# Kernel optimization log

Measured on AMD Instinct MI355X. Metric: run time of the kernel, lower is better.

Reference implementation:

```python
import jax, jax.numpy as jnp
import numpy as np

B, P, C = 64, 196, 768   # batch, num_patches, hidden_size
HS = 384                 # hidden_s (token-mixing hidden dim)
NG = 8                   # num_grids
GMIN, GMAX = -1.0, 1.0


def _rbf(x):
    # fast-KAN radial basis: exp(-((x - grid_i)/denom)^2), grid over [GMIN, GMAX]
    grid = jnp.linspace(GMIN, GMAX, NG).astype(x.dtype)
    denom = (GMAX - GMIN) / (NG - 1)
    return jnp.exp(-jnp.square((x[..., None] - grid) / denom))  # [..., din, NG]


def _kan_linear(x, spline_w, base_w, base_b):
    # x: [..., din]; spline_w: [dout, din*NG]; base_w: [dout, din]; base_b: [dout]
    basis = _rbf(x).reshape(*x.shape[:-1], -1)          # [..., din*NG]
    out = basis @ spline_w.T                            # spline term (no bias)
    out = out + jax.nn.silu(x) @ base_w.T + base_b      # base update term
    return out


def setup_inputs() -> dict:
    key = jax.random.key(0)
    ks = jax.random.split(key, 5)
    s = 0.1  # spline_weight_init_scale
    return {
        "x": jax.random.normal(ks[0], (B, P, C), jnp.float32),
        "fc1_spline_w": jax.random.normal(ks[1], (HS, P * NG), jnp.float32) * (s / np.sqrt(P * NG)),
        "fc1_base_w": jax.random.normal(ks[2], (HS, P), jnp.float32) / np.sqrt(P),
        "fc1_base_b": jnp.zeros((HS,), jnp.float32),
        "fc2_spline_w": jax.random.normal(ks[3], (P, HS * NG), jnp.float32) * (s / np.sqrt(HS * NG)),
        "fc2_base_w": jax.random.normal(ks[4], (P, HS), jnp.float32) / np.sqrt(HS),
        "fc2_base_b": jnp.zeros((P,), jnp.float32),
    }


def reference(x, fc1_spline_w, fc1_base_w, fc1_base_b,
              fc2_spline_w, fc2_base_w, fc2_base_b):
    skip_param = 1.0
    # token mixing: permute so KANLinear acts over the patch axis
    h = jnp.swapaxes(x, 1, 2)                                   # [B, C, P]
    h = _kan_linear(h, fc1_spline_w, fc1_base_w, fc1_base_b)    # [B, C, HS]
    # dropout p=0 -> identity; the two intermediate permutes cancel
    h = _kan_linear(h, fc2_spline_w, fc2_base_w, fc2_base_b)    # [B, C, P]
    out = jnp.swapaxes(h, 1, 2)                                 # [B, P, C]
    return out + skip_param * x
```

## Files before the change

### kernel.cpp

```cpp
#include <hip/hip_runtime.h>
#include <cstdint>

#define B_  64
#define P_  196
#define C_  768
#define HS_ 384
#define M_  49152
#define RT_ 96
#define NB_ (M_ / RT_)

#define NC1 13
#define KT1 111
#define NT1 12
#define NC2 24
#define KT2 216
#define NT2 7

#define H1_ELEMS  ((size_t)M_ * HS_)
#define W1P_ELEMS ((size_t)KT1 * NT1 * 512)
#define W2P_ELEMS ((size_t)KT2 * NT2 * 512)
#define PACK_G1   (W1P_ELEMS / 8)
#define PACK_G    ((W1P_ELEMS + W2P_ELEMS) / 8)

typedef __attribute__((ext_vector_type(8)))  short short8;
typedef __attribute__((ext_vector_type(16))) float f32x16;
typedef __attribute__((ext_vector_type(2)))  float float2v;

#define MFMA(w, a, c) __builtin_amdgcn_mfma_f32_32x32x16_bf16((w), (a), (c), 0, 0, 0)

static __device__ __forceinline__ float bf2f(unsigned short u) {
    union { unsigned int i; float f; } v; v.i = ((unsigned int)u) << 16; return v.f;
}
static __device__ __forceinline__ unsigned short f2bf_rne(float f) {
    union { float f; unsigned int i; } v; v.f = f;
    unsigned int r = v.i + 0x7FFFu + ((v.i >> 16) & 1u);
    return (unsigned short)(r >> 16);
}
static __device__ __forceinline__ unsigned int pack2(float a, float b) {
    unsigned int ua = __float_as_uint(a) + 0x8000u;
    unsigned int ub = __float_as_uint(b) + 0x8000u;
    return __builtin_amdgcn_perm(ub, ua, 0x07060302u);
}
static __device__ __forceinline__ short8 rbf8(float s) {
    const float Rr = 1.2011224087864498f;
    const float Aa = 4.2039284307525743f;
    float t1 = __builtin_fmaf(Aa, s, Aa);
    float2v t2 = {t1, t1};
    union { short8 s8; unsigned int u[4]; } r;
#pragma unroll
    for (int q = 0; q < 4; q++) {
        float2v c = {(float)(2 * q) * Rr, (float)(2 * q + 1) * Rr};
        float2v u = t2 - c;
        float2v m = -(u * u);
        r.u[q] = pack2(__builtin_amdgcn_exp2f(m[0]),
                       __builtin_amdgcn_exp2f(m[1]));
    }
    return r.s8;
}
static __device__ __forceinline__ unsigned int silu2(float a, float b) {
    const float L2E = 1.4426950408889634f;
    float2v v = {a, b};
    float2v t = v * (-L2E);
    float2v e = {__builtin_amdgcn_exp2f(t[0]), __builtin_amdgcn_exp2f(t[1])};
    float2v den = e + (float2v){1.f, 1.f};
    float2v rc = {__builtin_amdgcn_rcpf(den[0]), __builtin_amdgcn_rcpf(den[1])};
    float2v f = v * rc;
    return pack2(f[0], f[1]);
}

static __device__ __forceinline__ void block_sync_lds() {
    __builtin_amdgcn_sched_barrier(0);
    asm volatile("s_waitcnt lgkmcnt(0)" ::: "memory");
    __builtin_amdgcn_s_barrier();
    __builtin_amdgcn_sched_barrier(0);
}

static __device__ __forceinline__ void cvt8(const float4 a, const float4 b,
                                            unsigned short* o) {
    o[0] = f2bf_rne(a.x); o[1] = f2bf_rne(a.y); o[2] = f2bf_rne(a.z); o[3] = f2bf_rne(a.w);
    o[4] = f2bf_rne(b.x); o[5] = f2bf_rne(b.y); o[6] = f2bf_rne(b.z); o[7] = f2bf_rne(b.w);
}

__global__ void pack_w_kernel(const float* __restrict__ w1s,
                              const float* __restrict__ w1b,
                              const float* __restrict__ w2s,
                              const float* __restrict__ w2b,
                              unsigned short* __restrict__ w1p,
                              unsigned short* __restrict__ w2p) {
    int g = blockIdx.x * 256 + threadIdx.x;
    if (g >= PACK_G) return;
    union { short8 s8; unsigned short u[8]; } ov;
    if (g < PACK_G1) {
        int lane = g & 63;
        int lin  = g >> 6;
        int nt   = lin % NT1;
        int tt   = lin / NT1;
        int cc   = (tt < 108) ? tt / 9 : 12;
        int kk   = (tt < 108) ? tt % 9 : (tt - 108);
        int ktl  = (cc < 12) ? kk : ((kk < 2) ? kk : 8);
        int n = nt * 32 + (lane & 31);
        int khalf = lane >> 5;
        if (ktl < 8) {
            int p = cc * 16 + ktl * 2 + khalf;
            const float4* src = (const float4*)(w1s + (size_t)n * 1568 + (size_t)p * 8);
            cvt8(src[0], src[1], ov.u);
        } else {
            int p0 = cc * 16 + khalf * 8;
            if (p0 + 7 < P_) {
                const float4* src = (const float4*)(w1b + (size_t)n * 196 + p0);
                cvt8(src[0], src[1], ov.u);
            } else {
#pragma unroll
                for (int j = 0; j < 8; j++) {
                    int p = p0 + j;
                    float v = (p < P_) ? w1b[(size_t)n * 196 + p] : 0.f;
                    ov.u[j] = f2bf_rne(v);
                }
            }
        }
        *(short8*)&w1p[(size_t)g * 8] = ov.s8;
    } else {
        int g2 = g - PACK_G1;
        int lane = g2 & 63;
        int lin  = g2 >> 6;
        int nt   = lin % NT2;
        int tt   = lin / NT2;
        int cc   = tt / 9;
        int ktl  = tt % 9;
        int n = nt * 32 + (lane & 31);
        int khalf = lane >> 5;
        if (n < P_) {
            if (ktl < 8) {
                int s = cc * 16 + ktl * 2 + khalf;
                const float4* src = (const float4*)(w2s + (size_t)n * 3072 + (size_t)s * 8);
                cvt8(src[0], src[1], ov.u);
            } else {
                int s0 = cc * 16 + khalf * 8;
                const float4* src = (const float4*)(w2b + (size_t)n * 384 + s0);
                cvt8(src[0], src[1], ov.u);
            }
        } else {
#pragma unroll
            for (int j = 0; j < 8; j++) ov.u[j] = f2bf_rne(0.f);
        }
        *(short8*)&w2p[(size_t)g2 * 8] = ov.s8;
    }
}

#define TS_  1536
#define FB_  (9 * TS_)

__global__ __launch_bounds__(256, 2)
void fc1_kernel(const float* __restrict__ x,
                const unsigned short* __restrict__ w1p,
                const float* __restrict__ b1,
                unsigned short* __restrict__ h1t) {
    __shared__ __align__(16) unsigned short frag[2 * FB_];
    int blk = blockIdx.x;
    int tid = threadIdx.x;
    int b   = blk >> 3;
    int c0  = (blk & 7) * RT_;
    const float* xb = x + (size_t)b * (P_ * C_);

    int colA = tid & 63, scA = tid >> 6;
    int colB = 64 + (tid & 31), scB = tid >> 5;
    int pbase_rbfA  = ((colA >> 5) << 9) + (colA & 31) * 8;
    int pbase_rbfB  = 1024 + (colB & 31) * 8;
    int pbase_siluA = 8 * TS_ + ((colA >> 5) << 9) + ((scA >> 1) << 8) + (colA & 31) * 8 + (scA & 1) * 4;
    int pbase_siluB = 8 * TS_ + 1024 + ((scB >> 2) << 8) + (colB & 31) * 8 + (scB & 3) * 2;

    int wave = tid >> 6, lane = tid & 63;
    int l31 = lane & 31, half = lane >> 5;
    int nt0 = wave * 3;

    f32x16 acc[3][3];
#pragma unroll
    for (int rt = 0; rt < 3; rt++)
#pragma unroll
        for (int nt = 0; nt < 3; nt++)
#pragma unroll
            for (int i = 0; i < 16; i++) acc[rt][nt][i] = 0.f;

    const short8* wp = (const short8*)w1p;
    short8 wbuf[2][3];

    auto wload = [&](int d, const short8* wt0, int kk) {
        const short8* wt = wt0 + (size_t)kk * (NT1 * 64);
        wbuf[d][0] = wt[0]; wbuf[d][1] = wt[64]; wbuf[d][2] = wt[128];
    };
    auto do_mfma = [&](short8 w0, short8 w1, short8 w2,
                       short8 a0, short8 a1, short8 a2) {
        acc[0][0] = MFMA(w0, a0, acc[0][0]); acc[1][0] = MFMA(w0, a1, acc[1][0]); acc[2][0] = MFMA(w0, a2, acc[2][0]);
        acc[0][1] = MFMA(w1, a0, acc[0][1]); acc[1][1] = MFMA(w1, a1, acc[1][1]); acc[2][1] = MFMA(w1, a2, acc[2][1]);
        acc[0][2] = MFMA(w2, a0, acc[0][2]); acc[1][2] = MFMA(w2, a1, acc[1][2]); acc[2][2] = MFMA(w2, a2, acc[2][2]);
    };
    auto produce = [&](int fb, const float (&ra)[4], const float (&rb2)[2]) {
#pragma unroll
        for (int i = 0; i < 4; i++) {
            int sl = scA * 4 + i;
            *(short8*)&frag[fb + (sl >> 1) * TS_ + ((sl & 1) << 8) + pbase_rbfA] = rbf8(ra[i]);
        }
#pragma unroll
        for (int i = 0; i < 2; i++) {
            int sl = scB * 2 + i;
            *(short8*)&frag[fb + (sl >> 1) * TS_ + ((sl & 1) << 8) + pbase_rbfB] = rbf8(rb2[i]);
        }
        uint2 sv;
        sv.x = silu2(ra[0], ra[1]);
        sv.y = silu2(ra[2], ra[3]);
        *(uint2*)&frag[fb + pbase_siluA] = sv;
        *(unsigned int*)&frag[fb + pbase_siluB] = silu2(rb2[0], rb2[1]);
    };
    auto body = [&](int cc, const float (&rbPA)[4], const float (&rbPB)[2],
                    float (&rbLA)[4], float (&rbLB)[2]) {
        const short8* wt0 = wp + ((size_t)(cc * 9) * NT1 + nt0) * 64 + lane;
        wload(0, wt0, 0); wload(1, wt0, 1);
        int fbP = ((cc + 1) & 1) * FB_;
        const unsigned short* fg = &frag[(cc & 1) * FB_];
        short8 a0 = *(const short8*)&fg[lane * 8];
        short8 a1 = *(const short8*)&fg[512 + lane * 8];
        short8 a2 = *(const short8*)&fg[1024 + lane * 8];
#pragma unroll
        for (int kk = 0; kk < 9; kk++) {
            short8 na0, na1, na2;
            if (kk < 8) {
                na0 = *(const short8*)&fg[(kk + 1) * TS_ + lane * 8];
                na1 = *(const short8*)&fg[(kk + 1) * TS_ + 512 + lane * 8];
                na2 = *(const short8*)&fg[(kk + 1) * TS_ + 1024 + lane * 8];
            }
            short8 w0 = wbuf[kk & 1][0], w1 = wbuf[kk & 1][1], w2 = wbuf[kk & 1][2];
            if (kk < 7) wload(kk & 1, wt0, kk + 2);
            if (kk < 4) {
                int sl = scA * 4 + kk;
                *(short8*)&frag[fbP + (sl >> 1) * TS_ + ((sl & 1) << 8) + pbase_rbfA] = rbf8(rbPA[kk]);
            } else if (kk == 4) {
#pragma unroll
                for (int i = 0; i < 2; i++) {
                    int sl = scB * 2 + i;
                    *(short8*)&frag[fbP + (sl >> 1) * TS_ + ((sl & 1) << 8) + pbase_rbfB] = rbf8(rbPB[i]);
                }
            } else if (kk == 5) {
                uint2 sv;
                sv.x = silu2(rbPA[0], rbPA[1]);
                sv.y = silu2(rbPA[2], rbPA[3]);
                *(uint2*)&frag[fbP + pbase_siluA] = sv;
                *(unsigned int*)&frag[fbP + pbase_siluB] = silu2(rbPB[0], rbPB[1]);
            } else if (kk == 6) {
#pragma unroll
                for (int i = 0; i < 2; i++) {
                    int p = (cc + 2) * 16 + scA * 4 + i;
                    p = (p < P_) ? p : (P_ - 1);
                    rbLA[i] = xb[(size_t)p * C_ + c0 + colA];
                }
            } else if (kk == 7) {
#pragma unroll
                for (int i = 2; i < 4; i++) {
                    int p = (cc + 2) * 16 + scA * 4 + i;
                    p = (p < P_) ? p : (P_ - 1);
                    rbLA[i] = xb[(size_t)p * C_ + c0 + colA];
                }
            } else {
#pragma unroll
                for (int i = 0; i < 2; i++) {
                    int p = (cc + 2) * 16 + scB * 2 + i;
                    p = (p < P_) ? p : (P_ - 1);
                    rbLB[i] = xb[(size_t)p * C_ + c0 + colB];
                }
            }
            do_mfma(w0, w1, w2, a0, a1, a2);
            if (kk < 8) { a0 = na0; a1 = na1; a2 = na2; }
        }
        block_sync_lds();
    };

    float rbA_A[4], rbB_A[4], rbA_B[2], rbB_B[2];
#pragma unroll
    for (int i = 0; i < 4; i++) {
        rbA_A[i] = xb[(size_t)(scA * 4 + i) * C_ + c0 + colA];
        rbB_A[i] = xb[(size_t)(16 + scA * 4 + i) * C_ + c0 + colA];
    }
#pragma unroll
    for (int i = 0; i < 2; i++) {
        rbA_B[i] = xb[(size_t)(scB * 2 + i) * C_ + c0 + colB];
        rbB_B[i] = xb[(size_t)(16 + scB * 2 + i) * C_ + c0 + colB];
    }
    produce(0, rbA_A, rbA_B);
    block_sync_lds();

    for (int c2 = 0; c2 < 6; c2++) {
        body(2 * c2,     rbB_A, rbB_B, rbA_A, rbA_B);
        body(2 * c2 + 1, rbA_A, rbA_B, rbB_A, rbB_B);
    }
    {
        const short8* wt0 = wp + ((size_t)108 * NT1 + nt0) * 64 + lane;
        wload(0, wt0, 0); wload(1, wt0, 1);
        const unsigned short* fg = &frag[0];
#pragma unroll
        for (int kk = 0; kk < 3; kk++) {
            short8 w0 = wbuf[kk & 1][0], w1 = wbuf[kk & 1][1], w2 = wbuf[kk & 1][2];
            if (kk == 0) wload(0, wt0, 2);
            int ktl = (kk < 2) ? kk : 8;
            short8 a0 = *(const short8*)&fg[ktl * TS_ + lane * 8];
            short8 a1 = *(const short8*)&fg[ktl * TS_ + 512 + lane * 8];
            short8 a2 = *(const short8*)&fg[ktl * TS_ + 1024 + lane * 8];
            do_mfma(w0, w1, w2, a0, a1, a2);
        }
    }

#pragma unroll
    for (int nt = 0; nt < 3; nt++) {
        int n0 = (nt0 + nt) * 32 + 4 * half;
#pragma unroll
        for (int reg = 0; reg < 16; reg++) {
            int n = n0 + (reg & 3) + 8 * (reg >> 2);
            float bv = b1[n];
#pragma unroll
            for (int rt = 0; rt < 3; rt++) {
                h1t[(size_t)n * M_ + blk * RT_ + rt * 32 + l31] = f2bf_rne(acc[rt][nt][reg] + bv);
            }
        }
    }
}

__global__ __launch_bounds__(256, 2)
void fc2_kernel(const unsigned short* __restrict__ h1t,
                const unsigned short* __restrict__ w2p,
                const float* __restrict__ b2,
                const float* __restrict__ x,
                float* __restrict__ out) {
    __shared__ __align__(16) unsigned short frag[2 * FB_];
    int blk = blockIdx.x;
    int tid = threadIdx.x;
    int rbase = blk * RT_;

    int colA = tid & 63, scA = tid >> 6;
    int colB = 64 + (tid & 31), scB = tid >> 5;
    int pbase_rbfA  = ((colA >> 5) << 9) + (colA & 31) * 8;
    int pbase_rbfB  = 1024 + (colB & 31) * 8;
    int pbase_siluA = 8 * TS_ + ((colA >> 5) << 9) + ((scA >> 1) << 8) + (colA & 31) * 8 + (scA & 1) * 4;
    int pbase_siluB = 8 * TS_ + 1024 + ((scB >> 2) << 8) + (colB & 31) * 8 + (scB & 3) * 2;

    int wave = tid >> 6, lane = tid & 63;
    int l31 = lane & 31, half = lane >> 5;
    int nt0 = wave * 2;
    int ntn = (wave < 3) ? 2 : 1;
    int off1 = (ntn > 1) ? 64 : 0;

    f32x16 acc[3][2];
#pragma unroll
    for (int rt = 0; rt < 3; rt++)
#pragma unroll
        for (int nt = 0; nt < 2; nt++)
#pragma unroll
            for (int i = 0; i < 16; i++) acc[rt][nt][i] = 0.f;

    const short8* wp = (const short8*)w2p;
    short8 wbuf[2][2];

    auto wload = [&](int d, const short8* wt0, int kk) {
        const short8* wt = wt0 + (size_t)kk * (NT2 * 64);
        wbuf[d][0] = wt[0]; wbuf[d][1] = wt[off1];
    };
    auto do_mfma = [&](short8 w0, short8 w1, short8 a0, short8 a1, short8 a2) {
        acc[0][0] = MFMA(w0, a0, acc[0][0]); acc[1][0] = MFMA(w0, a1, acc[1][0]); acc[2][0] = MFMA(w0, a2, acc[2][0]);
        if (ntn == 2) {
            acc[0][1] = MFMA(w1, a0, acc[0][1]); acc[1][1] = MFMA(w1, a1, acc[1][1]); acc[2][1] = MFMA(w1, a2, acc[2][1]);
        }
    };
    auto produce = [&](int fb, const unsigned short (&ra)[4], const unsigned short (&rb2)[2]) {
        float v0 = bf2f(ra[0]), v1 = bf2f(ra[1]), v2 = bf2f(ra[2]), v3 = bf2f(ra[3]);
        float u0 = bf2f(rb2[0]), u1 = bf2f(rb2[1]);
        float vv[4] = {v0, v1, v2, v3};
#pragma unroll
        for (int i = 0; i < 4; i++) {
            int sl = scA * 4 + i;
            *(short8*)&frag[fb + (sl >> 1) * TS_ + ((sl & 1) << 8) + pbase_rbfA] = rbf8(vv[i]);
        }
        float uu[2] = {u0, u1};
#pragma unroll
        for (int i = 0; i < 2; i++) {
            int sl = scB * 2 + i;
            *(short8*)&frag[fb + (sl >> 1) * TS_ + ((sl & 1) << 8) + pbase_rbfB] = rbf8(uu[i]);
        }
        uint2 sv;
        sv.x = silu2(v0, v1);
        sv.y = silu2(v2, v3);
        *(uint2*)&frag[fb + pbase_siluA] = sv;
        *(unsigned int*)&frag[fb + pbase_siluB] = silu2(u0, u1);
    };
    auto body = [&](int cc, const unsigned short (&rbPA)[4], const unsigned short (&rbPB)[2],
                    unsigned short (&rbLA)[4], unsigned short (&rbLB)[2]) {
        bool doProd = (cc + 1 < NC2);
        const short8* wt0 = wp + ((size_t)(cc * 9) * NT2 + nt0) * 64 + lane;
        wload(0, wt0, 0); wload(1, wt0, 1);
        int fbP = ((cc + 1) & 1) * FB_;
        const unsigned short* fg = &frag[(cc & 1) * FB_];
        short8 a0 = *(const short8*)&fg[lane * 8];
        short8 a1 = *(const short8*)&fg[512 + lane * 8];
        short8 a2 = *(const short8*)&fg[1024 + lane * 8];
#pragma unroll
        for (int kk = 0; kk < 9; kk++) {
            short8 na0, na1, na2;
            if (kk < 8) {
                na0 = *(const short8*)&fg[(kk + 1) * TS_ + lane * 8];
                na1 = *(const short8*)&fg[(kk + 1) * TS_ + 512 + lane * 8];
                na2 = *(const short8*)&fg[(kk + 1) * TS_ + 1024 + lane * 8];
            }
            short8 w0 = wbuf[kk & 1][0], w1 = wbuf[kk & 1][1];
            if (kk < 7) wload(kk & 1, wt0, kk + 2);
            if (kk < 4) {
                if (doProd) {
                    int sl = scA * 4 + kk;
                    *(short8*)&frag[fbP + (sl >> 1) * TS_ + ((sl & 1) << 8) + pbase_rbfA] =
                        rbf8(bf2f(rbPA[kk]));
                }
            } else if (kk == 4) {
                if (doProd) {
#pragma unroll
                    for (int i = 0; i < 2; i++) {
                        int sl = scB * 2 + i;
                        *(short8*)&frag[fbP + (sl >> 1) * TS_ + ((sl & 1) << 8) + pbase_rbfB] =
                            rbf8(bf2f(rbPB[i]));
                    }
                }
            } else if (kk == 5) {
                if (doProd) {
                    uint2 sv;
                    sv.x = silu2(bf2f(rbPA[0]), bf2f(rbPA[1]));
                    sv.y = silu2(bf2f(rbPA[2]), bf2f(rbPA[3]));
                    *(uint2*)&frag[fbP + pbase_siluA] = sv;
                    *(unsigned int*)&frag[fbP + pbase_siluB] = silu2(bf2f(rbPB[0]), bf2f(rbPB[1]));
                }
            } else if (kk == 6) {
#pragma unroll
                for (int i = 0; i < 2; i++) {
                    int s = (cc + 2) * 16 + scA * 4 + i;
                    s = (s < HS_) ? s : (HS_ - 1);
                    rbLA[i] = h1t[(size_t)s * M_ + rbase + colA];
                }
            } else if (kk == 7) {
#pragma unroll
                for (int i = 2; i < 4; i++) {
                    int s = (cc + 2) * 16 + scA * 4 + i;
                    s = (s < HS_) ? s : (HS_ - 1);
                    rbLA[i] = h1t[(size_t)s * M_ + rbase + colA];
                }
            } else {
#pragma unroll
                for (int i = 0; i < 2; i++) {
                    int s = (cc + 2) * 16 + scB * 2 + i;
                    s = (s < HS_) ? s : (HS_ - 1);
                    rbLB[i] = h1t[(size_t)s * M_ + rbase + colB];
                }
            }
            do_mfma(w0, w1, a0, a1, a2);
            if (kk < 8) { a0 = na0; a1 = na1; a2 = na2; }
        }
        block_sync_lds();
    };

    unsigned short rbA_A[4], rbB_A[4], rbA_B[2], rbB_B[2];
#pragma unroll
    for (int i = 0; i < 4; i++) {
        rbA_A[i] = h1t[(size_t)(scA * 4 + i) * M_ + rbase + colA];
        rbB_A[i] = h1t[(size_t)(16 + scA * 4 + i) * M_ + rbase + colA];
    }
#pragma unroll
    for (int i = 0; i < 2; i++) {
        rbA_B[i] = h1t[(size_t)(scB * 2 + i) * M_ + rbase + colB];
        rbB_B[i] = h1t[(size_t)(16 + scB * 2 + i) * M_ + rbase + colB];
    }
    produce(0, rbA_A, rbA_B);
    block_sync_lds();

    for (int c2 = 0; c2 < 12; c2++) {
        body(2 * c2,     rbB_A, rbB_B, rbA_A, rbA_B);
        body(2 * c2 + 1, rbA_A, rbA_B, rbB_A, rbB_B);
    }

    int b = blk >> 3;
    int c0 = (blk & 7) * RT_;
#pragma unroll
    for (int nt = 0; nt < 2; nt++) {
        if (nt < ntn) {
            int p0 = (nt0 + nt) * 32 + 4 * half;
#pragma unroll
            for (int reg = 0; reg < 16; reg++) {
                int p = p0 + (reg & 3) + 8 * (reg >> 2);
                if (p < P_) {
                    float bv = b2[p];
#pragma unroll
                    for (int rt = 0; rt < 3; rt++) {
                        size_t off = ((size_t)b * P_ + p) * C_ + c0 + rt * 32 + l31;
                        out[off] = acc[rt][nt][reg] + bv + x[off];
                    }
                }
            }
        }
    }
}

extern "C" void kernel_launch(void* const* d_in, const int* in_sizes, int n_in,
                              void* d_out, int out_size, void* d_ws, size_t ws_size,
                              hipStream_t stream) {
    const float* x   = (const float*)d_in[0];
    const float* w1s = (const float*)d_in[1];
    const float* w1b = (const float*)d_in[2];
    const float* b1  = (const float*)d_in[3];
    const float* w2s = (const float*)d_in[4];
    const float* w2b = (const float*)d_in[5];
    const float* b2  = (const float*)d_in[6];
    float* out = (float*)d_out;

    unsigned short* h1t = (unsigned short*)d_ws;
    unsigned short* w1p = h1t + H1_ELEMS;
    unsigned short* w2p = w1p + W1P_ELEMS;

    int pack_blocks = (PACK_G + 255) / 256;
    pack_w_kernel<<<pack_blocks, 256, 0, stream>>>(w1s, w1b, w2s, w2b, w1p, w2p);
    fc1_kernel<<<NB_, 256, 0, stream>>>(x, w1p, b1, h1t);
    fc2_kernel<<<NB_, 256, 0, stream>>>(h1t, w2p, b2, x, out);
}
```

Before: 245.9 us.

## Fuse fc1 and fc2 into one kernel per row tile

Merges the two KAN layer kernels into a single kernel. Each block computes its 96-row slice of h1, writes it to global memory, waits with a vmcnt drain and barrier, then rereads that same slice for the fc2 stage. This removes one launch and the gap between kernels, and lets fc2 read recently written h1 data that may still be in cache. The price is higher register pressure from holding both stages in one kernel, which could lower occupancy. The rbf and silu helpers are also rewritten from float2 vectors to scalar arithmetic.

```diff
diff --git a/kernel.cpp b/kernel.cpp
--- a/kernel.cpp
+++ b/kernel.cpp
@@ -24,7 +24,6 @@
 
 typedef __attribute__((ext_vector_type(8)))  short short8;
 typedef __attribute__((ext_vector_type(16))) float f32x16;
-typedef __attribute__((ext_vector_type(2)))  float float2v;
 
 #define MFMA(w, a, c) __builtin_amdgcn_mfma_f32_32x32x16_bf16((w), (a), (c), 0, 0, 0)
 
@@ -45,27 +44,21 @@
     const float Rr = 1.2011224087864498f;
     const float Aa = 4.2039284307525743f;
     float t1 = __builtin_fmaf(Aa, s, Aa);
-    float2v t2 = {t1, t1};
     union { short8 s8; unsigned int u[4]; } r;
 #pragma unroll
     for (int q = 0; q < 4; q++) {
-        float2v c = {(float)(2 * q) * Rr, (float)(2 * q + 1) * Rr};
-        float2v u = t2 - c;
-        float2v m = -(u * u);
-        r.u[q] = pack2(__builtin_amdgcn_exp2f(m[0]),
-                       __builtin_amdgcn_exp2f(m[1]));
+        float u0 = t1 - (float)(2 * q) * Rr;
+        float u1 = t1 - (float)(2 * q + 1) * Rr;
+        r.u[q] = pack2(__builtin_amdgcn_exp2f(-u0 * u0),
+                       __builtin_amdgcn_exp2f(-u1 * u1));
     }
     return r.s8;
 }
 static __device__ __forceinline__ unsigned int silu2(float a, float b) {
     const float L2E = 1.4426950408889634f;
-    float2v v = {a, b};
-    float2v t = v * (-L2E);
-    float2v e = {__builtin_amdgcn_exp2f(t[0]), __builtin_amdgcn_exp2f(t[1])};
-    float2v den = e + (float2v){1.f, 1.f};
-    float2v rc = {__builtin_amdgcn_rcpf(den[0]), __builtin_amdgcn_rcpf(den[1])};
-    float2v f = v * rc;
-    return pack2(f[0], f[1]);
+    float fa = a * __builtin_amdgcn_rcpf(1.f + __builtin_amdgcn_exp2f(-L2E * a));
+    float fb = b * __builtin_amdgcn_rcpf(1.f + __builtin_amdgcn_exp2f(-L2E * b));
+    return pack2(fa, fb);
 }
 
 static __device__ __forceinline__ void block_sync_lds() {
@@ -151,15 +144,19 @@
 #define FB_  (9 * TS_)
 
 __global__ __launch_bounds__(256, 2)
-void fc1_kernel(const float* __restrict__ x,
-                const unsigned short* __restrict__ w1p,
-                const float* __restrict__ b1,
-                unsigned short* __restrict__ h1t) {
+void fc12_kernel(const float* __restrict__ x,
+                 const unsigned short* __restrict__ w1p,
+                 const float* __restrict__ b1,
+                 const unsigned short* __restrict__ w2p,
+                 const float* __restrict__ b2,
+                 unsigned short* __restrict__ h1t,
+                 float* __restrict__ out) {
     __shared__ __align__(16) unsigned short frag[2 * FB_];
     int blk = blockIdx.x;
     int tid = threadIdx.x;
     int b   = blk >> 3;
     int c0  = (blk & 7) * RT_;
+    int rbase = blk * RT_;
     const float* xb = x + (size_t)b * (P_ * C_);
 
     int colA = tid & 63, scA = tid >> 6;
@@ -171,328 +168,312 @@
 
     int wave = tid >> 6, lane = tid & 63;
     int l31 = lane & 31, half = lane >> 5;
-    int nt0 = wave * 3;
-
-    f32x16 acc[3][3];
-#pragma unroll
-    for (int rt = 0; rt < 3; rt++)
-#pragma unroll
-        for (int nt = 0; nt < 3; nt++)
-#pragma unroll
-            for (int i = 0; i < 16; i++) acc[rt][nt][i] = 0.f;
-
-    const short8* wp = (const short8*)w1p;
-    short8 wbuf[2][3];
-
-    auto wload = [&](int d, const short8* wt0, int kk) {
-        const short8* wt = wt0 + (size_t)kk * (NT1 * 64);
-        wbuf[d][0] = wt[0]; wbuf[d][1] = wt[64]; wbuf[d][2] = wt[128];
-    };
-    auto do_mfma = [&](short8 w0, short8 w1, short8 w2,
-                       short8 a0, short8 a1, short8 a2) {
-        acc[0][0] = MFMA(w0, a0, acc[0][0]); acc[1][0] = MFMA(w0, a1, acc[1][0]); acc[2][0] = MFMA(w0, a2, acc[2][0]);
-        acc[0][1] = MFMA(w1, a0, acc[0][1]); acc[1][1] = MFMA(w1, a1, acc[1][1]); acc[2][1] = MFMA(w1, a2, acc[2][1]);
-        acc[0][2] = MFMA(w2, a0, acc[0][2]); acc[1][2] = MFMA(w2, a1, acc[1][2]); acc[2][2] = MFMA(w2, a2, acc[2][2]);
-    };
-    auto produce = [&](int fb, const float (&ra)[4], const float (&rb2)[2]) {
-#pragma unroll
-        for (int i = 0; i < 4; i++) {
-            int sl = scA * 4 + i;
-            *(short8*)&frag[fb + (sl >> 1) * TS_ + ((sl & 1) << 8) + pbase_rbfA] = rbf8(ra[i]);
-        }
-#pragma unroll
-        for (int i = 0; i < 2; i++) {
-            int sl = scB * 2 + i;
-            *(short8*)&frag[fb + (sl >> 1) * TS_ + ((sl & 1) << 8) + pbase_rbfB] = rbf8(rb2[i]);
-        }
-        uint2 sv;
-        sv.x = silu2(ra[0], ra[1]);
-        sv.y = silu2(ra[2], ra[3]);
-        *(uint2*)&frag[fb + pbase_siluA] = sv;
-        *(unsigned int*)&frag[fb + pbase_siluB] = silu2(rb2[0], rb2[1]);
-    };
-    auto body = [&](int cc, const float (&rbPA)[4], const float (&rbPB)[2],
-                    float (&rbLA)[4], float (&rbLB)[2]) {
-        const short8* wt0 = wp + ((size_t)(cc * 9) * NT1 + nt0) * 64 + lane;
-        wload(0, wt0, 0); wload(1, wt0, 1);
-        int fbP = ((cc + 1) & 1) * FB_;
-        const unsigned short* fg = &frag[(cc & 1) * FB_];
-        short8 a0 = *(const short8*)&fg[lane * 8];
-        short8 a1 = *(const short8*)&fg[512 + lane * 8];
-        short8 a2 = *(const short8*)&fg[1024 + lane * 8];
-#pragma unroll
-        for (int kk = 0; kk < 9; kk++) {
-            short8 na0, na1, na2;
-            if (kk < 8) {
-                na0 = *(const short8*)&fg[(kk + 1) * TS_ + lane * 8];
-                na1 = *(const short8*)&fg[(kk + 1) * TS_ + 512 + lane * 8];
-                na2 = *(const short8*)&fg[(kk + 1) * TS_ + 1024 + lane * 8];
-            }
-            short8 w0 = wbuf[kk & 1][0], w1 = wbuf[kk & 1][1], w2 = wbuf[kk & 1][2];
-            if (kk < 7) wload(kk & 1, wt0, kk + 2);
-            if (kk < 4) {
-                int sl = scA * 4 + kk;
-                *(short8*)&frag[fbP + (sl >> 1) * TS_ + ((sl & 1) << 8) + pbase_rbfA] = rbf8(rbPA[kk]);
-            } else if (kk == 4) {
-#pragma unroll
-                for (int i = 0; i < 2; i++) {
-                    int sl = scB * 2 + i;
-                    *(short8*)&frag[fbP + (sl >> 1) * TS_ + ((sl & 1) << 8) + pbase_rbfB] = rbf8(rbPB[i]);
-                }
-            } else if (kk == 5) {
-                uint2 sv;
-                sv.x = silu2(rbPA[0], rbPA[1]);
-                sv.y = silu2(rbPA[2], rbPA[3]);
-                *(uint2*)&frag[fbP + pbase_siluA] = sv;
-                *(unsigned int*)&frag[fbP + pbase_siluB] = silu2(rbPB[0], rbPB[1]);
-            } else if (kk == 6) {
-#pragma unroll
-                for (int i = 0; i < 2; i++) {
-                    int p = (cc + 2) * 16 + scA * 4 + i;
-                    p = (p < P_) ? p : (P_ - 1);
-                    rbLA[i] = xb[(size_t)p * C_ + c0 + colA];
-                }
-            } else if (kk == 7) {
-#pragma unroll
-                for (int i = 2; i < 4; i++) {
-                    int p = (cc + 2) * 16 + scA * 4 + i;
-                    p = (p < P_) ? p : (P_ - 1);
-                    rbLA[i] = xb[(size_t)p * C_ + c0 + colA];
-                }
-            } else {
-#pragma unroll
-                for (int i = 0; i < 2; i++) {
-                    int p = (cc + 2) * 16 + scB * 2 + i;
-                    p = (p < P_) ? p : (P_ - 1);
-                    rbLB[i] = xb[(size_t)p * C_ + c0 + colB];
-                }
-            }
-            do_mfma(w0, w1, w2, a0, a1, a2);
-            if (kk < 8) { a0 = na0; a1 = na1; a2 = na2; }
-        }
-        block_sync_lds();
-    };
-
-    float rbA_A[4], rbB_A[4], rbA_B[2], rbB_B[2];
-#pragma unroll
-    for (int i = 0; i < 4; i++) {
-        rbA_A[i] = xb[(size_t)(scA * 4 + i) * C_ + c0 + colA];
-        rbB_A[i] = xb[(size_t)(16 + scA * 4 + i) * C_ + c0 + colA];
-    }
-#pragma unroll
-    for (int i = 0; i < 2; i++) {
-        rbA_B[i] = xb[(size_t)(scB * 2 + i) * C_ + c0 + colB];
-        rbB_B[i] = xb[(size_t)(16 + scB * 2 + i) * C_ + c0 + colB];
-    }
-    produce(0, rbA_A, rbA_B);
-    block_sync_lds();
-
-    for (int c2 = 0; c2 < 6; c2++) {
-        body(2 * c2,     rbB_A, rbB_B, rbA_A, rbA_B);
-        body(2 * c2 + 1, rbA_A, rbA_B, rbB_A, rbB_B);
-    }
+
     {
-        const short8* wt0 = wp + ((size_t)108 * NT1 + nt0) * 64 + lane;
-        wload(0, wt0, 0); wload(1, wt0, 1);
-        const unsigned short* fg = &frag[0];
-#pragma unroll
-        for (int kk = 0; kk < 3; kk++) {
-            short8 w0 = wbuf[kk & 1][0], w1 = wbuf[kk & 1][1], w2 = wbuf[kk & 1][2];
-            if (kk == 0) wload(0, wt0, 2);
-            int ktl = (kk < 2) ? kk : 8;
-            short8 a0 = *(const short8*)&fg[ktl * TS_ + lane * 8];
-            short8 a1 = *(const short8*)&fg[ktl * TS_ + 512 + lane * 8];
-            short8 a2 = *(const short8*)&fg[ktl * TS_ + 1024 + lane * 8];
-            do_mfma(w0, w1, w2, a0, a1, a2);
-        }
-    }
-
-#pragma unroll
-    for (int nt = 0; nt < 3; nt++) {
-        int n0 = (nt0 + nt) * 32 + 4 * half;
-#pragma unroll
-        for (int reg = 0; reg < 16; reg++) {
-            int n = n0 + (reg & 3) + 8 * (reg >> 2);
-            float bv = b1[n];
-#pragma unroll
-            for (int rt = 0; rt < 3; rt++) {
-                h1t[(size_t)n * M_ + blk * RT_ + rt * 32 + l31] = f2bf_rne(acc[rt][nt][reg] + bv);
-            }
-        }
-    }
-}
-
-__global__ __launch_bounds__(256, 2)
-void fc2_kernel(const unsigned short* __restrict__ h1t,
-                const unsigned short* __restrict__ w2p,
-                const float* __restrict__ b2,
-                const float* __restrict__ x,
-                float* __restrict__ out) {
-    __shared__ __align__(16) unsigned short frag[2 * FB_];
-    int blk = blockIdx.x;
-    int tid = threadIdx.x;
-    int rbase = blk * RT_;
-
-    int colA = tid & 63, scA = tid >> 6;
-    int colB = 64 + (tid & 31), scB = tid >> 5;
-    int pbase_rbfA  = ((colA >> 5) << 9) + (colA & 31) * 8;
-    int pbase_rbfB  = 1024 + (colB & 31) * 8;
-    int pbase_siluA = 8 * TS_ + ((colA >> 5) << 9) + ((scA >> 1) << 8) + (colA & 31) * 8 + (scA & 1) * 4;
-    int pbase_siluB = 8 * TS_ + 1024 + ((scB >> 2) << 8) + (colB & 31) * 8 + (scB & 3) * 2;
-
-    int wave = tid >> 6, lane = tid & 63;
-    int l31 = lane & 31, half = lane >> 5;
-    int nt0 = wave * 2;
-    int ntn = (wave < 3) ? 2 : 1;
-    int off1 = (ntn > 1) ? 64 : 0;
-
-    f32x16 acc[3][2];
-#pragma unroll
-    for (int rt = 0; rt < 3; rt++)
-#pragma unroll
-        for (int nt = 0; nt < 2; nt++)
-#pragma unroll
-            for (int i = 0; i < 16; i++) acc[rt][nt][i] = 0.f;
-
-    const short8* wp = (const short8*)w2p;
-    short8 wbuf[2][2];
-
-    auto wload = [&](int d, const short8* wt0, int kk) {
-        const short8* wt = wt0 + (size_t)kk * (NT2 * 64);
-        wbuf[d][0] = wt[0]; wbuf[d][1] = wt[off1];
-    };
-    auto do_mfma = [&](short8 w0, short8 w1, short8 a0, short8 a1, short8 a2) {
-        acc[0][0] = MFMA(w0, a0, acc[0][0]); acc[1][0] = MFMA(w0, a1, acc[1][0]); acc[2][0] = MFMA(w0, a2, acc[2][0]);
-        if (ntn == 2) {
+        int nt0 = wave * 3;
+        f32x16 acc[3][3];
+#pragma unroll
+        for (int rt = 0; rt < 3; rt++)
+#pragma unroll
+            for (int nt = 0; nt < 3; nt++)
+#pragma unroll
+                for (int i = 0; i < 16; i++) acc[rt][nt][i] = 0.f;
+
+        const short8* wp = (const short8*)w1p;
+        short8 wbuf[2][3];
+
+        auto wload = [&](int d, const short8* wt0, int kk) {
+            const short8* wt = wt0 + (size_t)kk * (NT1 * 64);
+            wbuf[d][0] = wt[0]; wbuf[d][1] = wt[64]; wbuf[d][2] = wt[128];
+        };
+        auto do_mfma = [&](short8 w0, short8 w1, short8 w2,
+                           short8 a0, short8 a1, short8 a2) {
+            acc[0][0] = MFMA(w0, a0, acc[0][0]); acc[1][0] = MFMA(w0, a1, acc[1][0]); acc[2][0] = MFMA(w0, a2, acc[2][0]);
             acc[0][1] = MFMA(w1, a0, acc[0][1]); acc[1][1] = MFMA(w1, a1, acc[1][1]); acc[2][1] = MFMA(w1, a2, acc[2][1]);
-        }
-    };
-    auto produce = [&](int fb, const unsigned short (&ra)[4], const unsigned short (&rb2)[2]) {
-        float v0 = bf2f(ra[0]), v1 = bf2f(ra[1]), v2 = bf2f(ra[2]), v3 = bf2f(ra[3]);
-        float u0 = bf2f(rb2[0]), u1 = bf2f(rb2[1]);
-        float vv[4] = {v0, v1, v2, v3};
-#pragma unroll
-        for (int i = 0; i < 4; i++) {
-            int sl = scA * 4 + i;
-            *(short8*)&frag[fb + (sl >> 1) * TS_ + ((sl & 1) << 8) + pbase_rbfA] = rbf8(vv[i]);
-        }
-        float uu[2] = {u0, u1};
-#pragma unroll
-        for (int i = 0; i < 2; i++) {
-            int sl = scB * 2 + i;
-            *(short8*)&frag[fb + (sl >> 1) * TS_ + ((sl & 1) << 8) + pbase_rbfB] = rbf8(uu[i]);
-        }
-        uint2 sv;
-        sv.x = silu2(v0, v1);
-        sv.y = silu2(v2, v3);
-        *(uint2*)&frag[fb + pbase_siluA] = sv;
-        *(unsigned int*)&frag[fb + pbase_siluB] = silu2(u0, u1);
-    };
-    auto body = [&](int cc, const unsigned short (&rbPA)[4], const unsigned short (&rbPB)[2],
-                    unsigned short (&rbLA)[4], unsigned short (&rbLB)[2]) {
-        bool doProd = (cc + 1 < NC2);
-        const short8* wt0 = wp + ((size_t)(cc * 9) * NT2 + nt0) * 64 + lane;
-        wload(0, wt0, 0); wload(1, wt0, 1);
-        int fbP = ((cc + 1) & 1) * FB_;
-        const unsigned short* fg = &frag[(cc & 1) * FB_];
-        short8 a0 = *(const short8*)&fg[lane * 8];
-        short8 a1 = *(const short8*)&fg[512 + lane * 8];
-        short8 a2 = *(const short8*)&fg[1024 + lane * 8];
-#pragma unroll
-        for (int kk = 0; kk < 9; kk++) {
-            short8 na0, na1, na2;
-            if (kk < 8) {
-                na0 = *(const short8*)&fg[(kk + 1) * TS_ + lane * 8];
-                na1 = *(const short8*)&fg[(kk + 1) * TS_ + 512 + lane * 8];
-                na2 = *(const short8*)&fg[(kk + 1) * TS_ + 1024 + lane * 8];
-            }
-            short8 w0 = wbuf[kk & 1][0], w1 = wbuf[kk & 1][1];
-            if (kk < 7) wload(kk & 1, wt0, kk + 2);
-            if (kk < 4) {
-                if (doProd) {
+            acc[0][2] = MFMA(w2, a0, acc[0][2]); acc[1][2] = MFMA(w2, a1, acc[1][2]); acc[2][2] = MFMA(w2, a2, acc[2][2]);
+        };
+        auto produce = [&](int fb, const float (&ra)[4], const float (&rb2)[2]) {
+#pragma unroll
+            for (int i = 0; i < 4; i++) {
+                int sl = scA * 4 + i;
+                *(short8*)&frag[fb + (sl >> 1) * TS_ + ((sl & 1) << 8) + pbase_rbfA] = rbf8(ra[i]);
+            }
+#pragma unroll
+            for (int i = 0; i < 2; i++) {
+                int sl = scB * 2 + i;
+                *(short8*)&frag[fb + (sl >> 1) * TS_ + ((sl & 1) << 8) + pbase_rbfB] = rbf8(rb2[i]);
+            }
+            uint2 sv;
+            sv.x = silu2(ra[0], ra[1]);
+            sv.y = silu2(ra[2], ra[3]);
+            *(uint2*)&frag[fb + pbase_siluA] = sv;
+            *(unsigned int*)&frag[fb + pbase_siluB] = silu2(rb2[0], rb2[1]);
+        };
+        auto body = [&](int cc, const float (&rbPA)[4], const float (&rbPB)[2],
+                        float (&rbLA)[4], float (&rbLB)[2]) {
+            const short8* wt0 = wp + ((size_t)(cc * 9) * NT1 + nt0) * 64 + lane;
+            wload(0, wt0, 0); wload(1, wt0, 1);
+            int fbP = ((cc + 1) & 1) * FB_;
+            const unsigned short* fg = &frag[(cc & 1) * FB_];
+            short8 a0 = *(const short8*)&fg[lane * 8];
+            short8 a1 = *(const short8*)&fg[512 + lane * 8];
+            short8 a2 = *(const short8*)&fg[1024 + lane * 8];
+#pragma unroll
+            for (int kk = 0; kk < 9; kk++) {
+                short8 na0, na1, na2;
+                if (kk < 8) {
+                    na0 = *(const short8*)&fg[(kk + 1) * TS_ + lane * 8];
+                    na1 = *(const short8*)&fg[(kk + 1) * TS_ + 512 + lane * 8];
+                    na2 = *(const short8*)&fg[(kk + 1) * TS_ + 1024 + lane * 8];
+                }
+                short8 w0 = wbuf[kk & 1][0], w1 = wbuf[kk & 1][1], w2 = wbuf[kk & 1][2];
+                if (kk < 7) wload(kk & 1, wt0, kk + 2);
+                if (kk < 4) {
                     int sl = scA * 4 + kk;
-                    *(short8*)&frag[fbP + (sl >> 1) * TS_ + ((sl & 1) << 8) + pbase_rbfA] =
-                        rbf8(bf2f(rbPA[kk]));
-                }
-            } else if (kk == 4) {
-                if (doProd) {
+                    *(short8*)&frag[fbP + (sl >> 1) * TS_ + ((sl & 1) << 8) + pbase_rbfA] = rbf8(rbPA[kk]);
+                } else if (kk == 4) {
 #pragma unroll
                     for (int i = 0; i < 2; i++) {
                         int sl = scB * 2 + i;
-                        *(short8*)&frag[fbP + (sl >> 1) * TS_ + ((sl & 1) << 8) + pbase_rbfB] =
-                            rbf8(bf2f(rbPB[i]));
-                    }
-                }
-            } else if (kk == 5) {
-                if (doProd) {
+                        *(short8*)&frag[fbP + (sl >> 1) * TS_ + ((sl & 1) << 8) + pbase_rbfB] = rbf8(rbPB[i]);
+                    }
+                } else if (kk == 5) {
                     uint2 sv;
-                    sv.x = silu2(bf2f(rbPA[0]), bf2f(rbPA[1]));
-                    sv.y = silu2(bf2f(rbPA[2]), bf2f(rbPA[3]));
+                    sv.x = silu2(rbPA[0], rbPA[1]);
+                    sv.y = silu2(rbPA[2], rbPA[3]);
                     *(uint2*)&frag[fbP + pbase_siluA] = sv;
-                    *(unsigned int*)&frag[fbP + pbase_siluB] = silu2(bf2f(rbPB[0]), bf2f(rbPB[1]));
-                }
-            } else if (kk == 6) {
-#pragma unroll
-                for (int i = 0; i < 2; i++) {
-                    int s = (cc + 2) * 16 + scA * 4 + i;
-                    s = (s < HS_) ? s : (HS_ - 1);
-                    rbLA[i] = h1t[(size_t)s * M_ + rbase + colA];
-                }
-            } else if (kk == 7) {
-#pragma unroll
-                for (int i = 2; i < 4; i++) {
-                    int s = (cc + 2) * 16 + scA * 4 + i;
-                    s = (s < HS_) ? s : (HS_ - 1);
-                    rbLA[i] = h1t[(size_t)s * M_ + rbase + colA];
-                }
-            } else {
-#pragma unroll
-                for (int i = 0; i < 2; i++) {
-                    int s = (cc + 2) * 16 + scB * 2 + i;
-                    s = (s < HS_) ? s : (HS_ - 1);
-                    rbLB[i] = h1t[(size_t)s * M_ + rbase + colB];
-                }
-            }
-            do_mfma(w0, w1, a0, a1, a2);
-            if (kk < 8) { a0 = na0; a1 = na1; a2 = na2; }
-        }
+                    *(unsigned int*)&frag[fbP + pbase_siluB] = silu2(rbPB[0], rbPB[1]);
+                } else if (kk == 6) {
+#pragma unroll
+                    for (int i = 0; i < 2; i++) {
+                        int p = (cc + 2) * 16 + scA * 4 + i;
+                        p = (p < P_) ? p : (P_ - 1);
+                        rbLA[i] = xb[(size_t)p * C_ + c0 + colA];
+                    }
+                } else if (kk == 7) {
+#pragma unroll
+                    for (int i = 2; i < 4; i++) {
+                        int p = (cc + 2) * 16 + scA * 4 + i;
+                        p = (p < P_) ? p : (P_ - 1);
+                        rbLA[i] = xb[(size_t)p * C_ + c0 + colA];
+                    }
+                } else {
+#pragma unroll
+                    for (int i = 0; i < 2; i++) {
+                        int p = (cc + 2) * 16 + scB * 2 + i;
+                        p = (p < P_) ? p : (P_ - 1);
+                        rbLB[i] = xb[(size_t)p * C_ + c0 + colB];
+                    }
+                }
+                do_mfma(w0, w1, w2, a0, a1, a2);
+                if (kk < 8) { a0 = na0; a1 = na1; a2 = na2; }
+            }
+            block_sync_lds();
+        };
+
+        float rbA_A[4], rbB_A[4], rbA_B[2], rbB_B[2];
+#pragma unroll
+        for (int i = 0; i < 4; i++) {
+            rbA_A[i] = xb[(size_t)(scA * 4 + i) * C_ + c0 + colA];
+            rbB_A[i] = xb[(size_t)(16 + scA * 4 + i) * C_ + c0 + colA];
+        }
+#pragma unroll
+        for (int i = 0; i < 2; i++) {
+            rbA_B[i] = xb[(size_t)(scB * 2 + i) * C_ + c0 + colB];
+            rbB_B[i] = xb[(size_t)(16 + scB * 2 + i) * C_ + c0 + colB];
+        }
+        produce(0, rbA_A, rbA_B);
         block_sync_lds();
-    };
-
-    unsigned short rbA_A[4], rbB_A[4], rbA_B[2], rbB_B[2];
-#pragma unroll
-    for (int i = 0; i < 4; i++) {
-        rbA_A[i] = h1t[(size_t)(scA * 4 + i) * M_ + rbase + colA];
-        rbB_A[i] = h1t[(size_t)(16 + scA * 4 + i) * M_ + rbase + colA];
+
+        for (int c2 = 0; c2 < 6; c2++) {
+            body(2 * c2,     rbB_A, rbB_B, rbA_A, rbA_B);
+            body(2 * c2 + 1, rbA_A, rbA_B, rbB_A, rbB_B);
+        }
+        {
+            const short8* wt0 = wp + ((size_t)108 * NT1 + nt0) * 64 + lane;
+            wload(0, wt0, 0); wload(1, wt0, 1);
+            const unsigned short* fg = &frag[0];
+#pragma unroll
+            for (int kk = 0; kk < 3; kk++) {
+                short8 w0 = wbuf[kk & 1][0], w1 = wbuf[kk & 1][1], w2 = wbuf[kk & 1][2];
+                if (kk == 0) wload(0, wt0, 2);
+                int ktl = (kk < 2) ? kk : 8;
+                short8 a0 = *(const short8*)&fg[ktl * TS_ + lane * 8];
+                short8 a1 = *(const short8*)&fg[ktl * TS_ + 512 + lane * 8];
+                short8 a2 = *(const short8*)&fg[ktl * TS_ + 1024 + lane * 8];
+                do_mfma(w0, w1, w2, a0, a1, a2);
+            }
+        }
+
+#pragma unroll
+        for (int nt = 0; nt < 3; nt++) {
+            int n0 = (nt0 + nt) * 32 + 4 * half;
+#pragma unroll
+            for (int reg = 0; reg < 16; reg++) {
+                int n = n0 + (reg & 3) + 8 * (reg >> 2);
+                float bv = b1[n];
+#pragma unroll
+                for (int rt = 0; rt < 3; rt++) {
+                    h1t[(size_t)n * M_ + blk * RT_ + rt * 32 + l31] = f2bf_rne(acc[rt][nt][reg] + bv);
+                }
+            }
+        }
     }
-#pragma unroll
-    for (int i = 0; i < 2; i++) {
-        rbA_B[i] = h1t[(size_t)(scB * 2 + i) * M_ + rbase + colB];
-        rbB_B[i] = h1t[(size_t)(16 + scB * 2 + i) * M_ + rbase + colB];
-    }
-    produce(0, rbA_A, rbA_B);
-    block_sync_lds();
-
-    for (int c2 = 0; c2 < 12; c2++) {
-        body(2 * c2,     rbB_A, rbB_B, rbA_A, rbA_B);
-        body(2 * c2 + 1, rbA_A, rbA_B, rbB_A, rbB_B);
-    }
-
-    int b = blk >> 3;
-    int c0 = (blk & 7) * RT_;
-#pragma unroll
-    for (int nt = 0; nt < 2; nt++) {
-        if (nt < ntn) {
-            int p0 = (nt0 + nt) * 32 + 4 * half;
-#pragma unroll
-            for (int reg = 0; reg < 16; reg++) {
-                int p = p0 + (reg & 3) + 8 * (reg >> 2);
-                if (p < P_) {
-                    float bv = b2[p];
-#pragma unroll
-                    for (int rt = 0; rt < 3; rt++) {
-                        size_t off = ((size_t)b * P_ + p) * C_ + c0 + rt * 32 + l31;
-                        out[off] = acc[rt][nt][reg] + bv + x[off];
+
+    asm volatile("s_waitcnt vmcnt(0)" ::: "memory");
+    __syncthreads();
+
+    {
+        int nt0 = wave * 2;
+        int ntn = (wave < 3) ? 2 : 1;
+        int off1 = (ntn > 1) ? 64 : 0;
+
+        f32x16 acc[3][2];
+#pragma unroll
+        for (int rt = 0; rt < 3; rt++)
+#pragma unroll
+            for (int nt = 0; nt < 2; nt++)
+#pragma unroll
+                for (int i = 0; i < 16; i++) acc[rt][nt][i] = 0.f;
+
+        const short8* wp = (const short8*)w2p;
+        short8 wbuf[2][2];
+
+        auto wload = [&](int d, const short8* wt0, int kk) {
+            const short8* wt = wt0 + (size_t)kk * (NT2 * 64);
+            wbuf[d][0] = wt[0]; wbuf[d][1] = wt[off1];
+        };
+        auto do_mfma = [&](short8 w0, short8 w1, short8 a0, short8 a1, short8 a2) {
+            acc[0][0] = MFMA(w0, a0, acc[0][0]); acc[1][0] = MFMA(w0, a1, acc[1][0]); acc[2][0] = MFMA(w0, a2, acc[2][0]);
+            if (ntn == 2) {
+                acc[0][1] = MFMA(w1, a0, acc[0][1]); acc[1][1] = MFMA(w1, a1, acc[1][1]); acc[2][1] = MFMA(w1, a2, acc[2][1]);
+            }
+        };
+        auto produce = [&](int fb, const unsigned short (&ra)[4], const unsigned short (&rb2)[2]) {
+            float v0 = bf2f(ra[0]), v1 = bf2f(ra[1]), v2 = bf2f(ra[2]), v3 = bf2f(ra[3]);
+            float u0 = bf2f(rb2[0]), u1 = bf2f(rb2[1]);
+            float vv[4] = {v0, v1, v2, v3};
+#pragma unroll
+            for (int i = 0; i < 4; i++) {
+                int sl = scA * 4 + i;
+                *(short8*)&frag[fb + (sl >> 1) * TS_ + ((sl & 1) << 8) + pbase_rbfA] = rbf8(vv[i]);
+            }
+            float uu[2] = {u0, u1};
+#pragma unroll
+            for (int i = 0; i < 2; i++) {
+                int sl = scB * 2 + i;
+                *(short8*)&frag[fb + (sl >> 1) * TS_ + ((sl & 1) << 8) + pbase_rbfB] = rbf8(uu[i]);
+            }
+            uint2 sv;
+            sv.x = silu2(v0, v1);
+            sv.y = silu2(v2, v3);
+            *(uint2*)&frag[fb + pbase_siluA] = sv;
+            *(unsigned int*)&frag[fb + pbase_siluB] = silu2(u0, u1);
+        };
+        auto body = [&](int cc, const unsigned short (&rbPA)[4], const unsigned short (&rbPB)[2],
+                        unsigned short (&rbLA)[4], unsigned short (&rbLB)[2]) {
+            bool doProd = (cc + 1 < NC2);
+            const short8* wt0 = wp + ((size_t)(cc * 9) * NT2 + nt0) * 64 + lane;
+            wload(0, wt0, 0); wload(1, wt0, 1);
+            int fbP = ((cc + 1) & 1) * FB_;
+            const unsigned short* fg = &frag[(cc & 1) * FB_];
+            short8 a0 = *(const short8*)&fg[lane * 8];
+            short8 a1 = *(const short8*)&fg[512 + lane * 8];
+            short8 a2 = *(const short8*)&fg[1024 + lane * 8];
+#pragma unroll
+            for (int kk = 0; kk < 9; kk++) {
+                short8 na0, na1, na2;
+                if (kk < 8) {
+                    na0 = *(const short8*)&fg[(kk + 1) * TS_ + lane * 8];
+                    na1 = *(const short8*)&fg[(kk + 1) * TS_ + 512 + lane * 8];
+                    na2 = *(const short8*)&fg[(kk + 1) * TS_ + 1024 + lane * 8];
+                }
+                short8 w0 = wbuf[kk & 1][0], w1 = wbuf[kk & 1][1];
+                if (kk < 7) wload(kk & 1, wt0, kk + 2);
+                if (kk < 4) {
+                    if (doProd) {
+                        int sl = scA * 4 + kk;
+                        *(short8*)&frag[fbP + (sl >> 1) * TS_ + ((sl & 1) << 8) + pbase_rbfA] =
+                            rbf8(bf2f(rbPA[kk]));
+                    }
+                } else if (kk == 4) {
+                    if (doProd) {
+#pragma unroll
+                        for (int i = 0; i < 2; i++) {
+                            int sl = scB * 2 + i;
+                            *(short8*)&frag[fbP + (sl >> 1) * TS_ + ((sl & 1) << 8) + pbase_rbfB] =
+                                rbf8(bf2f(rbPB[i]));
+                        }
+                    }
+                } else if (kk == 5) {
+                    if (doProd) {
+                        uint2 sv;
+                        sv.x = silu2(bf2f(rbPA[0]), bf2f(rbPA[1]));
+                        sv.y = silu2(bf2f(rbPA[2]), bf2f(rbPA[3]));
+                        *(uint2*)&frag[fbP + pbase_siluA] = sv;
+                        *(unsigned int*)&frag[fbP + pbase_siluB] = silu2(bf2f(rbPB[0]), bf2f(rbPB[1]));
+                    }
+                } else if (kk == 6) {
+#pragma unroll
+                    for (int i = 0; i < 2; i++) {
+                        int s = (cc + 2) * 16 + scA * 4 + i;
+                        s = (s < HS_) ? s : (HS_ - 1);
+                        rbLA[i] = h1t[(size_t)s * M_ + rbase + colA];
+                    }
+                } else if (kk == 7) {
+#pragma unroll
+                    for (int i = 2; i < 4; i++) {
+                        int s = (cc + 2) * 16 + scA * 4 + i;
+                        s = (s < HS_) ? s : (HS_ - 1);
+                        rbLA[i] = h1t[(size_t)s * M_ + rbase + colA];
+                    }
+                } else {
+#pragma unroll
+                    for (int i = 0; i < 2; i++) {
+                        int s = (cc + 2) * 16 + scB * 2 + i;
+                        s = (s < HS_) ? s : (HS_ - 1);
+                        rbLB[i] = h1t[(size_t)s * M_ + rbase + colB];
+                    }
+                }
+                do_mfma(w0, w1, a0, a1, a2);
+                if (kk < 8) { a0 = na0; a1 = na1; a2 = na2; }
+            }
+            block_sync_lds();
+        };
+
+        unsigned short rbA_A[4], rbB_A[4], rbA_B[2], rbB_B[2];
+#pragma unroll
+        for (int i = 0; i < 4; i++) {
+            rbA_A[i] = h1t[(size_t)(scA * 4 + i) * M_ + rbase + colA];
+            rbB_A[i] = h1t[(size_t)(16 + scA * 4 + i) * M_ + rbase + colA];
+        }
+#pragma unroll
+        for (int i = 0; i < 2; i++) {
+            rbA_B[i] = h1t[(size_t)(scB * 2 + i) * M_ + rbase + colB];
+            rbB_B[i] = h1t[(size_t)(16 + scB * 2 + i) * M_ + rbase + colB];
+        }
+        produce(0, rbA_A, rbA_B);
+        block_sync_lds();
+
+        for (int c2 = 0; c2 < 12; c2++) {
+            body(2 * c2,     rbB_A, rbB_B, rbA_A, rbA_B);
+            body(2 * c2 + 1, rbA_A, rbA_B, rbB_A, rbB_B);
+        }
+
+#pragma unroll
+        for (int nt = 0; nt < 2; nt++) {
+            if (nt < ntn) {
+                int p0 = (nt0 + nt) * 32 + 4 * half;
+#pragma unroll
+                for (int reg = 0; reg < 16; reg++) {
+                    int p = p0 + (reg & 3) + 8 * (reg >> 2);
+                    if (p < P_) {
+                        float bv = b2[p];
+#pragma unroll
+                        for (int rt = 0; rt < 3; rt++) {
+                            size_t off = ((size_t)b * P_ + p) * C_ + c0 + rt * 32 + l31;
+                            out[off] = acc[rt][nt][reg] + bv + x[off];
+                        }
                     }
                 }
             }
@@ -518,6 +499,5 @@
 
     int pack_blocks = (PACK_G + 255) / 256;
     pack_w_kernel<<<pack_blocks, 256, 0, stream>>>(w1s, w1b, w2s, w2b, w1p, w2p);
-    fc1_kernel<<<NB_, 256, 0, stream>>>(x, w1p, b1, h1t);
-    fc2_kernel<<<NB_, 256, 0, stream>>>(h1t, w2p, b2, x, out);
-}
+    fc12_kernel<<<NB_, 256, 0, stream>>>(x, w1p, b1, w2p, b2, h1t, out);
+}
```

Result: no change. 245.3 us (-0.2%).
